# Kernel optimization log

Measured on AMD Instinct MI355X. Metric: run time of the kernel, lower is better.

## Reference

```python
import jax, jax.numpy as jnp
import numpy as np
import itertools

L, F, T = 16, 2, 2**19          # levels, features/level, hashmap size
BASE, SCALE = 16, 1.5           # base resolution, per-level scale
N = 524288                      # batch of sample points
PRIMES = np.array([1, 2654435761, 805459861, 3674653429], dtype=np.uint32)


def hash_encode(x, table):
    """Multi-resolution hash-grid encoding. x: [N,d] in [0,1); table: [L,T,F]."""
    n, d = x.shape
    corners = jnp.asarray(list(itertools.product([0, 1], repeat=d)), dtype=jnp.uint32)  # [C,d]
    primes = jnp.asarray(PRIMES[:d])
    is_hi = corners.astype(bool)[None]          # [1,C,d]
    outs = []
    for l in range(L):
        res = float(np.floor(BASE * SCALE**l))
        pos = x * res
        p0f = jnp.floor(pos)
        frac = pos - p0f                         # [N,d]
        p0 = p0f.astype(jnp.uint32)
        coords = p0[:, None, :] + corners[None]  # [N,C,d] uint32 (wraps)
        m = coords * primes                      # [N,C,d]
        h = m[..., 0]
        for j in range(1, d):
            h = h ^ m[..., j]
        idx = (h % np.uint32(T)).astype(jnp.int32)              # [N,C]
        w = jnp.where(is_hi, frac[:, None, :], 1.0 - frac[:, None, :]).prod(-1)  # [N,C]
        feat = table[l][idx]                                    # [N,C,F]
        outs.append(jnp.einsum('nc,ncf->nf', w, feat))
    return jnp.concatenate(outs, axis=-1)        # [N, L*F]


def mlp(h, w_in, w_hid, w_out):
    """tcnn-style bias-free MLP, ReLU hidden, linear output."""
    h = jax.nn.relu(h @ w_in)
    for i in range(w_hid.shape[0]):
        h = jax.nn.relu(h @ w_hid[i])
    return h @ w_out


def setup_inputs() -> dict:
    key = jax.random.key(0)
    ks = jax.random.split(key, 20)
    def w(k, shape):
        fan = shape[-2]
        return jax.random.normal(k, shape, jnp.float32) / np.sqrt(fan).astype(np.float32)
    return {
        'x': jax.random.uniform(ks[0], (N, 3), jnp.float32),
        't': jax.random.uniform(ks[1], (1,), jnp.float32),
        'skip_alpha': jax.random.uniform(ks[2], (1,), jnp.float32),
        'table_s': jax.random.normal(ks[3], (L, T, F), jnp.float32) * 1e-2,
        'ws_in': w(ks[4], (32, 64)),
        'ws_hid': w(ks[5], (3, 64, 64)),
        'ws_out': w(ks[6], (64, 64)),
        'table_d': jax.random.normal(ks[7], (L, T, F), jnp.float32) * 1e-2,
        'wd_in': w(ks[8], (32, 64)),
        'wd_hid': w(ks[9], (3, 64, 64)),
        'wd_out': w(ks[10], (64, 64)),
        'w1_in': w(ks[11], (128, 64)),
        'w1_hid': w(ks[12], (1, 64, 64)),
        'w1_out': w(ks[13], (64, 128)),
        'w2_in': w(ks[14], (128, 64)),
        'w2_hid': w(ks[15], (1, 64, 64)),
        'w2_out': w(ks[16], (64, 1)),
    }


def reference(x, t, skip_alpha, table_s, ws_in, ws_hid, ws_out,
              table_d, wd_in, wd_hid, wd_out,
              w1_in, w1_hid, w1_out, w2_in, w2_hid, w2_out):
    static_features = mlp(hash_encode(x, table_s), ws_in, ws_hid, ws_out)          # [N,64]
    t_col = jnp.broadcast_to(t, (x.shape[0], 1))
    x4 = jnp.concatenate([x, t_col], axis=1)                                        # [N,4]
    dynamic_features = mlp(hash_encode(x4, table_d), wd_in, wd_hid, wd_out)        # [N,64]
    features = jnp.concatenate([static_features, dynamic_features], axis=-1)       # [N,128]
    out1 = mlp(features, w1_in, w1_hid, w1_out)                                     # [N,128]
    blended = out1 * skip_alpha + (1.0 - skip_alpha) * features
    return mlp(blended, w2_in, w2_hid, w2_out)                                      # [N,1]
```

## Files before the change

### kernel.cpp

```cpp
#include <hip/hip_runtime.h>
#include <hip/hip_bf16.h>
#include <stdint.h>

#define LVLS 16
#define TSZ  524288
#define TMASK 0x7FFFFu
#define NPTS 524288
#define P1 2654435761u
#define P2 805459861u
#define P3 3674653429u

__constant__ float RES_TAB[16] = {
    16.f, 24.f, 36.f, 54.f, 81.f, 121.f, 182.f, 273.f,
    410.f, 615.f, 922.f, 1383.f, 2075.f, 3113.f, 4670.f, 7006.f};

using f16x8 = __attribute__((ext_vector_type(8))) _Float16;
using f32x4 = __attribute__((ext_vector_type(4))) float;
using u32x8 = __attribute__((ext_vector_type(8))) uint32_t;

union PackF16 { uint32_t u; _Float16 h[2]; };

constexpr int PS = 72;

struct WPtrs { const float* p[11]; };

__global__ void k_build(const float* __restrict__ ts, const float* __restrict__ td,
                        const float* __restrict__ tptr, uint2* __restrict__ Tc,
                        WPtrs wp, _Float16* __restrict__ wdst) {
    int B = blockIdx.x;
    int tid = threadIdx.x;
    if (B < 40960) {
        int c = B & 7, j = B >> 3;
        int l, i;
        if (j < 1024) {
            l = c >> 1;
            i = (c & 1) * 262144 + j * 256 + tid;
        } else if (j < 3072) {
            l = 12 + (c >> 1);
            i = (j - 1024) * 256 + tid;
        } else {
            l = 4 + c;
            i = (j - 3072) * 256 + tid;
        }
        int id = l * TSZ + i;
        float2 sv = ((const float2*)ts)[id];
        float res = RES_TAB[l];
        float tv  = tptr[0];
        float pt  = tv * res;
        float fpt = floorf(pt);
        float ft  = pt - fpt;
        uint32_t ut = (uint32_t)(int)fpt;
        uint32_t h0 = (ut * P3) & TMASK;
        uint32_t h1 = ((ut + 1u) * P3) & TMASK;
        const float2* tdl = (const float2*)td + (size_t)l * TSZ;
        float2 a = tdl[i ^ h0];
        float2 b = tdl[i ^ h1];
        PackF16 o0, o1;
        o0.h[0] = (_Float16)sv.x; o0.h[1] = (_Float16)sv.y;
        o1.h[0] = (_Float16)((1.f - ft) * a.x + ft * b.x);
        o1.h[1] = (_Float16)((1.f - ft) * a.y + ft * b.y);
        Tc[id] = make_uint2(o0.u, o1.u);
    } else {
        int id = (B - 40960) * 256 + tid;
        if (id >= 69632) return;
        const int OFF[16] = {0,2048,6144,10240,14336,18432,20480,24576,28672,
                             32768,36864,45056,49152,57344,65536,69632};
        const int KK[15]  = {32,64,64,64,64,32,64,64,64,64,128,64,64,128,64};
        const int NN[15]  = {64,64,64,64,64,64,64,64,64,64,64,64,128,64,64};
        const int PSEL[15]= {0,1,1,1,2,3,4,4,4,5,6,7,8,9,10};
        const int POFF[15]= {0,0,4096,8192,0,0,0,4096,8192,0,0,0,0,0,0};
        int m = 0;
        while (id >= OFF[m+1]) m++;
        int local = id - OFF[m];
        int jj   = local & 7;
        int lane = (local >> 3) & 63;
        int blk  = local >> 9;
        int KC   = KK[m] >> 5;
        int ct   = blk / KC;
        int kc   = blk - ct * KC;
        int k    = kc*32 + ((lane>>4)<<3) + jj;
        int n    = ct*16 + (lane & 15);
        const float* src = wp.p[PSEL[m]] + POFF[m];
        wdst[id] = (_Float16)src[k * NN[m] + n];
    }
}

__device__ __forceinline__ void gather1(const uint2* __restrict__ tcl,
                                        float px, float py, float pz,
                                        u32x8& va, u32x8& vb,
                                        float& wx, float& wy, float& wz) {
    float fx = floorf(px), fy = floorf(py), fz = floorf(pz);
    wx = px - fx; wy = py - fy; wz = pz - fz;
    uint32_t ux = (uint32_t)(int)fx, uy = (uint32_t)(int)fy, uz = (uint32_t)(int)fz;
    uint32_t hx0 = ux,     hx1 = ux + 1u;
    uint32_t hy0 = uy*P1,  hy1 = (uy+1u)*P1;
    uint32_t hz0 = uz*P2,  hz1 = (uz+1u)*P2;
#pragma unroll
    for (int cc = 0; cc < 8; cc++) {
        uint32_t idx = (((cc&1)?hx1:hx0) ^ ((cc&2)?hy1:hy0) ^ ((cc&4)?hz1:hz0)) & TMASK;
        uint2 t = tcl[idx];
        if (cc < 4) { va[(cc&3)*2+0] = t.x; va[(cc&3)*2+1] = t.y; }
        else        { vb[(cc&3)*2+0] = t.x; vb[(cc&3)*2+1] = t.y; }
    }
}

__device__ __forceinline__ void consume1(const u32x8& va, const u32x8& vb,
                                         float wx, float wy, float wz,
                                         uint32_t* __restrict__ es,
                                         uint32_t* __restrict__ ed, int p) {
    float wxa[2] = {1.f-wx, wx}, wya[2] = {1.f-wy, wy}, wza[2] = {1.f-wz, wz};
    float sA0 = 0.f, sA1 = 0.f, sD0 = 0.f, sD1 = 0.f;
#pragma unroll
    for (int cc = 0; cc < 8; cc++) {
        float w = wxa[cc&1] * wya[(cc>>1)&1] * wza[cc>>2];
        PackF16 s, d;
        s.u = (cc<4) ? va[(cc&3)*2+0] : vb[(cc&3)*2+0];
        d.u = (cc<4) ? va[(cc&3)*2+1] : vb[(cc&3)*2+1];
        sA0 += w*(float)s.h[0]; sA1 += w*(float)s.h[1];
        sD0 += w*(float)d.h[0]; sD1 += w*(float)d.h[1];
    }
    PackF16 o;
    o.h[0] = (_Float16)sA0; o.h[1] = (_Float16)sA1; es[p] = o.u;
    o.h[0] = (_Float16)sD0; o.h[1] = (_Float16)sD1; ed[p] = o.u;
}

#define MEMFENCE asm volatile("" ::: "memory")
#define PIN(a,b,c,d) asm volatile("" : "+v"(a), "+v"(b), "+v"(c), "+v"(d))

__launch_bounds__(256, 4)
__global__ void k_encode(const float* __restrict__ x,
                         const uint2* __restrict__ Tc,
                         uint32_t* __restrict__ EncS, uint32_t* __restrict__ EncD) {
    int tid = threadIdx.x;
    int c   = blockIdx.x & 7;
    int b   = blockIdx.x >> 3;
    int l, pb, stride;
    if (b < 256) {
        l = 4 + c;
        pb = b * 256 + tid;
        stride = 65536;
    } else if (b < 384) {
        l = 12 + (c >> 1);
        pb = (c & 1) * 262144 + (b - 256) * 256 + tid;
        stride = 32768;
    } else {
        l = c >> 1;
        pb = (c & 1) * 262144 + (b - 384) * 256 + tid;
        stride = 32768;
    }
    const uint2* tcl = Tc + (size_t)l * TSZ;
    uint32_t* es = EncS + (size_t)l * NPTS;
    uint32_t* ed = EncD + (size_t)l * NPTS;
    float res = RES_TAB[l];

    float PX[8], PY[8], PZ[8];
#pragma unroll
    for (int i = 0; i < 8; i++) {
        int p = pb + i * stride;
        PX[i] = x[p*3+0]*res; PY[i] = x[p*3+1]*res; PZ[i] = x[p*3+2]*res;
    }

    u32x8 A0, A1, A2, A3, B0, B1, B2, B3;
    float wA0x, wA0y, wA0z, wA1x, wA1y, wA1z;
    float wB0x, wB0y, wB0z, wB1x, wB1y, wB1z;

    gather1(tcl, PX[0], PY[0], PZ[0], A0, A1, wA0x, wA0y, wA0z);
    gather1(tcl, PX[1], PY[1], PZ[1], A2, A3, wA1x, wA1y, wA1z);
    gather1(tcl, PX[2], PY[2], PZ[2], B0, B1, wB0x, wB0y, wB0z);
    gather1(tcl, PX[3], PY[3], PZ[3], B2, B3, wB1x, wB1y, wB1z);
    MEMFENCE;
    PIN(A0, A1, A2, A3);
    consume1(A0, A1, wA0x, wA0y, wA0z, es, ed, pb + 0*stride);
    consume1(A2, A3, wA1x, wA1y, wA1z, es, ed, pb + 1*stride);
    gather1(tcl, PX[4], PY[4], PZ[4], A0, A1, wA0x, wA0y, wA0z);
    gather1(tcl, PX[5], PY[5], PZ[5], A2, A3, wA1x, wA1y, wA1z);
    MEMFENCE;
    PIN(B0, B1, B2, B3);
    consume1(B0, B1, wB0x, wB0y, wB0z, es, ed, pb + 2*stride);
    consume1(B2, B3, wB1x, wB1y, wB1z, es, ed, pb + 3*stride);
    gather1(tcl, PX[6], PY[6], PZ[6], B0, B1, wB0x, wB0y, wB0z);
    gather1(tcl, PX[7], PY[7], PZ[7], B2, B3, wB1x, wB1y, wB1z);
    MEMFENCE;
    PIN(A0, A1, A2, A3);
    consume1(A0, A1, wA0x, wA0y, wA0z, es, ed, pb + 4*stride);
    consume1(A2, A3, wA1x, wA1y, wA1z, es, ed, pb + 5*stride);
    PIN(B0, B1, B2, B3);
    consume1(B0, B1, wB0x, wB0y, wB0z, es, ed, pb + 6*stride);
    consume1(B2, B3, wB1x, wB1y, wB1z, es, ed, pb + 7*stride);
}

__device__ __forceinline__ void wait_lds() {
    asm volatile("s_waitcnt lgkmcnt(0)" ::: "memory");
}

template<int KC, bool RELU>
__device__ __forceinline__ void mm2(const f16x8 a[2][4], const f16x8* __restrict__ B,
                                    _Float16* dst, int m, int quad, int lane) {
#pragma unroll
    for (int ct = 0; ct < 4; ct++) {
        f32x4 acc0 = {0.f,0.f,0.f,0.f}, acc1 = {0.f,0.f,0.f,0.f};
#pragma unroll
        for (int kc = 0; kc < KC; kc++) {
            f16x8 b = B[(ct*KC+kc)*64 + lane];
            acc0 = __builtin_amdgcn_mfma_f32_16x16x32_f16(a[0][kc], b, acc0, 0, 0, 0);
            acc1 = __builtin_amdgcn_mfma_f32_16x16x32_f16(a[1][kc], b, acc1, 0, 0, 0);
        }
#pragma unroll
        for (int i = 0; i < 4; i++) {
            float v0 = acc0[i], v1 = acc1[i];
            if (RELU) { v0 = fmaxf(v0, 0.f); v1 = fmaxf(v1, 0.f); }
            dst[(0*16 + quad*4+i)*PS + ct*16 + m] = (_Float16)v0;
            dst[(1*16 + quad*4+i)*PS + ct*16 + m] = (_Float16)v1;
        }
    }
}

template<int KC>
__device__ __forceinline__ void mm2_keep(const f16x8 a[2][4], const f16x8* __restrict__ B,
                                         _Float16* dst, PackF16 P[2][8],
                                         int m, int quad, int lane) {
#pragma unroll
    for (int ct = 0; ct < 4; ct++) {
        f32x4 acc0 = {0.f,0.f,0.f,0.f}, acc1 = {0.f,0.f,0.f,0.f};
#pragma unroll
        for (int kc = 0; kc < KC; kc++) {
            f16x8 b = B[(ct*KC+kc)*64 + lane];
            acc0 = __builtin_amdgcn_mfma_f32_16x16x32_f16(a[0][kc], b, acc0, 0, 0, 0);
            acc1 = __builtin_amdgcn_mfma_f32_16x16x32_f16(a[1][kc], b, acc1, 0, 0, 0);
        }
#pragma unroll
        for (int ih = 0; ih < 2; ih++) {
            PackF16 p0, p1;
            p0.h[0] = (_Float16)acc0[ih*2+0]; p0.h[1] = (_Float16)acc0[ih*2+1];
            p1.h[0] = (_Float16)acc1[ih*2+0]; p1.h[1] = (_Float16)acc1[ih*2+1];
            P[0][ct*2+ih] = p0; P[1][ct*2+ih] = p1;
            dst[(0*16 + quad*4+ih*2+0)*PS + ct*16 + m] = p0.h[0];
            dst[(0*16 + quad*4+ih*2+1)*PS + ct*16 + m] = p0.h[1];
            dst[(1*16 + quad*4+ih*2+0)*PS + ct*16 + m] = p1.h[0];
            dst[(1*16 + quad*4+ih*2+1)*PS + ct*16 + m] = p1.h[1];
        }
    }
}

template<int KC>
__device__ __forceinline__ void read_a(const _Float16* buf, f16x8 a[2][4], int m, int quad) {
#pragma unroll
    for (int rt = 0; rt < 2; rt++)
#pragma unroll
        for (int kc = 0; kc < KC; kc++)
            a[rt][kc] = *(const f16x8*)(buf + (rt*16 + m)*PS + kc*32 + quad*8);
}

__device__ __forceinline__ void read_a128(const _Float16* Fs, const _Float16* Fd,
                                          f16x8 a[2][4], int m, int quad) {
#pragma unroll
    for (int rt = 0; rt < 2; rt++) {
#pragma unroll
        for (int kc = 0; kc < 2; kc++) {
            a[rt][kc]   = *(const f16x8*)(Fs + (rt*16 + m)*PS + kc*32 + quad*8);
            a[rt][kc+2] = *(const f16x8*)(Fd + (rt*16 + m)*PS + kc*32 + quad*8);
        }
    }
}

__device__ __forceinline__ void load_enc(const uint32_t* __restrict__ Enc,
                                         int pbase, int m, int quad, f16x8 a[2][4]) {
#pragma unroll
    for (int rt = 0; rt < 2; rt++) {
        union { uint32_t u[4]; f16x8 v; } cv;
        int p = pbase + rt*16 + m;
#pragma unroll
        for (int j = 0; j < 4; j++)
            cv.u[j] = Enc[(size_t)(quad*4 + j) * NPTS + p];
        a[rt][0] = cv.v;
    }
}

__launch_bounds__(256, 4)
__global__ void k_mlp(const uint32_t* __restrict__ EncS, const uint32_t* __restrict__ EncD,
                      const _Float16* __restrict__ Wfrag, const float* __restrict__ alphap,
                      const float* __restrict__ w2out, float* __restrict__ out) {
    __shared__ _Float16 FsB[4][32*PS];
    __shared__ _Float16 FdB[4][32*PS];
    int tid  = threadIdx.x;
    int wave = tid >> 6, lane = tid & 63;
    int m = lane & 15, quad = lane >> 4;
    int pbase = blockIdx.x * 128 + wave * 32;
    _Float16* Fs = FsB[wave];
    _Float16* Fd = FdB[wave];
    const f16x8* W8 = (const f16x8*)Wfrag;
    float alpha = alphap[0];

    f16x8 a[2][4];
    PackF16 sP[2][8], dP[2][8];

    load_enc(EncS, pbase, m, quad, a);
    mm2<1, true>(a, W8 + 0,    Fs, m, quad, lane); wait_lds();
    read_a<2>(Fs, a, m, quad);
    mm2<2, true>(a, W8 + 256,  Fs, m, quad, lane); wait_lds();
    read_a<2>(Fs, a, m, quad);
    mm2<2, true>(a, W8 + 768,  Fs, m, quad, lane); wait_lds();
    read_a<2>(Fs, a, m, quad);
    mm2<2, true>(a, W8 + 1280, Fs, m, quad, lane); wait_lds();
    read_a<2>(Fs, a, m, quad);
    mm2_keep<2>(a, W8 + 1792, Fs, sP, m, quad, lane);
    load_enc(EncD, pbase, m, quad, a);
    mm2<1, true>(a, W8 + 2304, Fd, m, quad, lane); wait_lds();
    read_a<2>(Fd, a, m, quad);
    mm2<2, true>(a, W8 + 2560, Fd, m, quad, lane); wait_lds();
    read_a<2>(Fd, a, m, quad);
    mm2<2, true>(a, W8 + 3072, Fd, m, quad, lane); wait_lds();
    read_a<2>(Fd, a, m, quad);
    mm2<2, true>(a, W8 + 3584, Fd, m, quad, lane); wait_lds();
    read_a<2>(Fd, a, m, quad);
    mm2_keep<2>(a, W8 + 4096, Fd, dP, m, quad, lane); wait_lds();
    read_a128(Fs, Fd, a, m, quad);
    mm2<4, true>(a, W8 + 4608, Fs, m, quad, lane); wait_lds();
    read_a<2>(Fs, a, m, quad);
    mm2<2, true>(a, W8 + 5632, Fs, m, quad, lane); wait_lds();
    read_a<2>(Fs, a, m, quad);
#pragma unroll
    for (int ct = 0; ct < 8; ct++) {
        f32x4 acc0 = {0.f,0.f,0.f,0.f}, acc1 = {0.f,0.f,0.f,0.f};
#pragma unroll
        for (int kc = 0; kc < 2; kc++) {
            f16x8 b = W8[6144 + (ct*2+kc)*64 + lane];
            acc0 = __builtin_amdgcn_mfma_f32_16x16x32_f16(a[0][kc], b, acc0, 0, 0, 0);
            acc1 = __builtin_amdgcn_mfma_f32_16x16x32_f16(a[1][kc], b, acc1, 0, 0, 0);
        }
        _Float16* tgt = (ct < 4) ? Fs : Fd;
        int col = (ct & 3) * 16 + m;
#pragma unroll
        for (int i = 0; i < 4; i++) {
            float f0 = (ct < 4) ? (float)sP[0][ct*2 + (i>>1)].h[i&1]
                                : (float)dP[0][(ct-4)*2 + (i>>1)].h[i&1];
            float f1 = (ct < 4) ? (float)sP[1][ct*2 + (i>>1)].h[i&1]
                                : (float)dP[1][(ct-4)*2 + (i>>1)].h[i&1];
            tgt[(0*16 + quad*4+i)*PS + col] = (_Float16)(alpha*acc0[i] + (1.f-alpha)*f0);
            tgt[(1*16 + quad*4+i)*PS + col] = (_Float16)(alpha*acc1[i] + (1.f-alpha)*f1);
        }
    }
    wait_lds();
    read_a128(Fs, Fd, a, m, quad);
    mm2<4, true>(a, W8 + 7168, Fs, m, quad, lane); wait_lds();
    read_a<2>(Fs, a, m, quad);
    float rsum0[4] = {0.f,0.f,0.f,0.f}, rsum1[4] = {0.f,0.f,0.f,0.f};
#pragma unroll
    for (int ct = 0; ct < 4; ct++) {
        f32x4 acc0 = {0.f,0.f,0.f,0.f}, acc1 = {0.f,0.f,0.f,0.f};
#pragma unroll
        for (int kc = 0; kc < 2; kc++) {
            f16x8 b = W8[8192 + (ct*2+kc)*64 + lane];
            acc0 = __builtin_amdgcn_mfma_f32_16x16x32_f16(a[0][kc], b, acc0, 0, 0, 0);
            acc1 = __builtin_amdgcn_mfma_f32_16x16x32_f16(a[1][kc], b, acc1, 0, 0, 0);
        }
        float wv = w2out[ct*16 + m];
#pragma unroll
        for (int i = 0; i < 4; i++) {
            rsum0[i] += fmaxf(acc0[i], 0.f) * wv;
            rsum1[i] += fmaxf(acc1[i], 0.f) * wv;
        }
    }
#pragma unroll
    for (int off = 1; off < 16; off <<= 1) {
#pragma unroll
        for (int i = 0; i < 4; i++) {
            rsum0[i] += __shfl_xor(rsum0[i], off, 64);
            rsum1[i] += __shfl_xor(rsum1[i], off, 64);
        }
    }
    if (m == 0) {
#pragma unroll
        for (int i = 0; i < 4; i++) {
            out[pbase + 0*16 + quad*4 + i] = rsum0[i];
            out[pbase + 1*16 + quad*4 + i] = rsum1[i];
        }
    }
}

extern "C" void kernel_launch(void* const* d_in, const int* in_sizes, int n_in,
                              void* d_out, int out_size, void* d_ws, size_t ws_size,
                              hipStream_t stream) {
    const float* x      = (const float*)d_in[0];
    const float* t      = (const float*)d_in[1];
    const float* alpha  = (const float*)d_in[2];
    const float* tab_s  = (const float*)d_in[3];
    const float* ws_in  = (const float*)d_in[4];
    const float* ws_hid = (const float*)d_in[5];
    const float* ws_out = (const float*)d_in[6];
    const float* tab_d  = (const float*)d_in[7];
    const float* wd_in  = (const float*)d_in[8];
    const float* wd_hid = (const float*)d_in[9];
    const float* wd_out = (const float*)d_in[10];
    const float* w1_in  = (const float*)d_in[11];
    const float* w1_hid = (const float*)d_in[12];
    const float* w1_out = (const float*)d_in[13];
    const float* w2_in  = (const float*)d_in[14];
    const float* w2_hid = (const float*)d_in[15];
    const float* w2_out = (const float*)d_in[16];
    float* out = (float*)d_out;

    char* ws = (char*)d_ws;
    _Float16* Wfrag = (_Float16*)ws;
    uint2*    Tc    = (uint2*)(ws + 139264);
    uint32_t* EncS  = (uint32_t*)(ws + 139264 + 67108864);
    uint32_t* EncD  = EncS + (size_t)LVLS * NPTS;
    size_t needed = 139264 + 67108864 + 2ull * 33554432ull;
    if (ws_size < needed) return;

    WPtrs wp;
    wp.p[0] = ws_in;  wp.p[1] = ws_hid; wp.p[2] = ws_out;
    wp.p[3] = wd_in;  wp.p[4] = wd_hid; wp.p[5] = wd_out;
    wp.p[6] = w1_in;  wp.p[7] = w1_hid; wp.p[8] = w1_out;
    wp.p[9] = w2_in;  wp.p[10] = w2_hid;

    k_build  <<<41232, 256, 0, stream>>>(tab_s, tab_d, t, Tc, wp, Wfrag);
    k_encode <<<4096,  256, 0, stream>>>(x, Tc, EncS, EncD);
    k_mlp    <<<NPTS/128, 256, 0, stream>>>(EncS, EncD, Wfrag, alpha, w2_out, out);
}
```

Baseline: 545.9 us.

## Pair x-adjacent hash corners into 16-byte loads with a three-deep gather pipeline

The encode gather now uses the fact that the x-neighbour corners differ only in the low hash bits. When ux is even, the two x-corners land in the same aligned 16-byte pair, so one uint4 load fetches both. When ux is odd, four extra 8-byte loads are issued. The software pipeline also changes from batches of 2+2 points to a rotating three-slot schedule, with x coordinates loaded inside each issue. This cuts load instructions and transactions for about half the points, at the cost of divergent branches on x-parity and extra select logic.

```diff
diff --git a/kernel.cpp b/kernel.cpp
--- a/kernel.cpp
+++ b/kernel.cpp
@@ -85,47 +85,86 @@
     }
 }
 
-__device__ __forceinline__ void gather1(const uint2* __restrict__ tcl,
-                                        float px, float py, float pz,
-                                        u32x8& va, u32x8& vb,
-                                        float& wx, float& wy, float& wz) {
+#define MEMFENCE asm volatile("" ::: "memory")
+#define PIN3(a,b,c) asm volatile("" : "+v"(a), "+v"(b), "+v"(c))
+
+__device__ __forceinline__ void issueP(const float* __restrict__ x,
+                                       const uint2* __restrict__ tcl, float res,
+                                       int p,
+                                       u32x8& vp0, u32x8& vp1, u32x8& vo,
+                                       float& wx, float& wy, float& wz,
+                                       uint32_t& sel, uint32_t& par) {
+    float px = x[p*3+0]*res, py = x[p*3+1]*res, pz = x[p*3+2]*res;
     float fx = floorf(px), fy = floorf(py), fz = floorf(pz);
-    wx = px - fx; wy = py - fy; wz = pz - fz;
+    wx = px-fx; wy = py-fy; wz = pz-fz;
     uint32_t ux = (uint32_t)(int)fx, uy = (uint32_t)(int)fy, uz = (uint32_t)(int)fz;
-    uint32_t hx0 = ux,     hx1 = ux + 1u;
-    uint32_t hy0 = uy*P1,  hy1 = (uy+1u)*P1;
-    uint32_t hz0 = uz*P2,  hz1 = (uz+1u)*P2;
-#pragma unroll
-    for (int cc = 0; cc < 8; cc++) {
-        uint32_t idx = (((cc&1)?hx1:hx0) ^ ((cc&2)?hy1:hy0) ^ ((cc&4)?hz1:hz0)) & TMASK;
-        uint2 t = tcl[idx];
-        if (cc < 4) { va[(cc&3)*2+0] = t.x; va[(cc&3)*2+1] = t.y; }
-        else        { vb[(cc&3)*2+0] = t.x; vb[(cc&3)*2+1] = t.y; }
-    }
-}
-
-__device__ __forceinline__ void consume1(const u32x8& va, const u32x8& vb,
+    uint32_t hy0 = uy*P1, hy1 = (uy+1u)*P1;
+    uint32_t hz0 = uz*P2, hz1 = (uz+1u)*P2;
+    par = ux & 1u;
+    if (par) {
+#pragma unroll
+        for (int d = 0; d < 4; d++) {
+            uint32_t r  = ((d&1) ? hy1 : hy0) ^ ((d>>1) ? hz1 : hz0);
+            uint32_t i1 = ((ux + 1u) ^ r) & TMASK;
+            uint2 t = tcl[i1];
+            vo[d*2+0] = t.x; vo[d*2+1] = t.y;
+        }
+    }
+    uint32_t s = 0;
+#pragma unroll
+    for (int d = 0; d < 4; d++) {
+        uint32_t r  = ((d&1) ? hy1 : hy0) ^ ((d>>1) ? hz1 : hz0);
+        uint32_t i0 = (ux ^ r) & TMASK;
+        s |= (i0 & 1u) << d;
+        const uint32_t* src = (const uint32_t*)tcl + (size_t)(i0 & ~1u) * 2u;
+        uint4 t = *(const uint4*)src;
+        if (d < 2) {
+            vp0[(d&1)*4+0] = t.x; vp0[(d&1)*4+1] = t.y;
+            vp0[(d&1)*4+2] = t.z; vp0[(d&1)*4+3] = t.w;
+        } else {
+            vp1[(d&1)*4+0] = t.x; vp1[(d&1)*4+1] = t.y;
+            vp1[(d&1)*4+2] = t.z; vp1[(d&1)*4+3] = t.w;
+        }
+    }
+    sel = s;
+}
+
+__device__ __forceinline__ void consumeP(const u32x8& vp0, const u32x8& vp1,
+                                         const u32x8& vo,
                                          float wx, float wy, float wz,
+                                         uint32_t sel, uint32_t par,
                                          uint32_t* __restrict__ es,
                                          uint32_t* __restrict__ ed, int p) {
     float wxa[2] = {1.f-wx, wx}, wya[2] = {1.f-wy, wy}, wza[2] = {1.f-wz, wz};
     float sA0 = 0.f, sA1 = 0.f, sD0 = 0.f, sD1 = 0.f;
-#pragma unroll
-    for (int cc = 0; cc < 8; cc++) {
-        float w = wxa[cc&1] * wya[(cc>>1)&1] * wza[cc>>2];
-        PackF16 s, d;
-        s.u = (cc<4) ? va[(cc&3)*2+0] : vb[(cc&3)*2+0];
-        d.u = (cc<4) ? va[(cc&3)*2+1] : vb[(cc&3)*2+1];
-        sA0 += w*(float)s.h[0]; sA1 += w*(float)s.h[1];
-        sD0 += w*(float)d.h[0]; sD1 += w*(float)d.h[1];
+    bool odd = (par != 0u);
+#pragma unroll
+    for (int d = 0; d < 4; d++) {
+        uint32_t h0 = (sel >> d) & 1u;
+        const int e = (d&1)*4;
+        uint32_t lo0 = (d<2) ? vp0[e+0] : vp1[e+0];
+        uint32_t lo1 = (d<2) ? vp0[e+1] : vp1[e+1];
+        uint32_t hi0 = (d<2) ? vp0[e+2] : vp1[e+2];
+        uint32_t hi1 = (d<2) ? vp0[e+3] : vp1[e+3];
+        uint32_t a0 = h0 ? hi0 : lo0;
+        uint32_t a1 = h0 ? hi1 : lo1;
+        uint32_t p0w = h0 ? lo0 : hi0;
+        uint32_t p1w = h0 ? lo1 : hi1;
+        uint32_t b0 = odd ? vo[d*2+0] : p0w;
+        uint32_t b1 = odd ? vo[d*2+1] : p1w;
+        float wyz = wya[d&1] * wza[d>>1];
+        float w0 = wxa[0]*wyz, w1 = wxa[1]*wyz;
+        PackF16 s0, d0, s1, d1;
+        s0.u = a0; d0.u = a1; s1.u = b0; d1.u = b1;
+        sA0 += w0*(float)s0.h[0] + w1*(float)s1.h[0];
+        sA1 += w0*(float)s0.h[1] + w1*(float)s1.h[1];
+        sD0 += w0*(float)d0.h[0] + w1*(float)d1.h[0];
+        sD1 += w0*(float)d0.h[1] + w1*(float)d1.h[1];
     }
     PackF16 o;
     o.h[0] = (_Float16)sA0; o.h[1] = (_Float16)sA1; es[p] = o.u;
     o.h[0] = (_Float16)sD0; o.h[1] = (_Float16)sD1; ed[p] = o.u;
 }
-
-#define MEMFENCE asm volatile("" ::: "memory")
-#define PIN(a,b,c,d) asm volatile("" : "+v"(a), "+v"(b), "+v"(c), "+v"(d))
 
 __launch_bounds__(256, 4)
 __global__ void k_encode(const float* __restrict__ x,
@@ -153,40 +192,41 @@
     uint32_t* ed = EncD + (size_t)l * NPTS;
     float res = RES_TAB[l];
 
-    float PX[8], PY[8], PZ[8];
-#pragma unroll
-    for (int i = 0; i < 8; i++) {
-        int p = pb + i * stride;
-        PX[i] = x[p*3+0]*res; PY[i] = x[p*3+1]*res; PZ[i] = x[p*3+2]*res;
-    }
-
-    u32x8 A0, A1, A2, A3, B0, B1, B2, B3;
-    float wA0x, wA0y, wA0z, wA1x, wA1y, wA1z;
-    float wB0x, wB0y, wB0z, wB1x, wB1y, wB1z;
-
-    gather1(tcl, PX[0], PY[0], PZ[0], A0, A1, wA0x, wA0y, wA0z);
-    gather1(tcl, PX[1], PY[1], PZ[1], A2, A3, wA1x, wA1y, wA1z);
-    gather1(tcl, PX[2], PY[2], PZ[2], B0, B1, wB0x, wB0y, wB0z);
-    gather1(tcl, PX[3], PY[3], PZ[3], B2, B3, wB1x, wB1y, wB1z);
-    MEMFENCE;
-    PIN(A0, A1, A2, A3);
-    consume1(A0, A1, wA0x, wA0y, wA0z, es, ed, pb + 0*stride);
-    consume1(A2, A3, wA1x, wA1y, wA1z, es, ed, pb + 1*stride);
-    gather1(tcl, PX[4], PY[4], PZ[4], A0, A1, wA0x, wA0y, wA0z);
-    gather1(tcl, PX[5], PY[5], PZ[5], A2, A3, wA1x, wA1y, wA1z);
-    MEMFENCE;
-    PIN(B0, B1, B2, B3);
-    consume1(B0, B1, wB0x, wB0y, wB0z, es, ed, pb + 2*stride);
-    consume1(B2, B3, wB1x, wB1y, wB1z, es, ed, pb + 3*stride);
-    gather1(tcl, PX[6], PY[6], PZ[6], B0, B1, wB0x, wB0y, wB0z);
-    gather1(tcl, PX[7], PY[7], PZ[7], B2, B3, wB1x, wB1y, wB1z);
-    MEMFENCE;
-    PIN(A0, A1, A2, A3);
-    consume1(A0, A1, wA0x, wA0y, wA0z, es, ed, pb + 4*stride);
-    consume1(A2, A3, wA1x, wA1y, wA1z, es, ed, pb + 5*stride);
-    PIN(B0, B1, B2, B3);
-    consume1(B0, B1, wB0x, wB0y, wB0z, es, ed, pb + 6*stride);
-    consume1(B2, B3, wB1x, wB1y, wB1z, es, ed, pb + 7*stride);
+    u32x8 pA0, pA1, pB0, pB1, pC0, pC1;
+    u32x8 oA = {}, oB = {}, oC = {};
+    float wAx, wAy, wAz, wBx, wBy, wBz, wCx, wCy, wCz;
+    uint32_t selA, parA, selB, parB, selC, parC;
+
+    issueP(x, tcl, res, pb + 0*stride, pA0, pA1, oA, wAx, wAy, wAz, selA, parA);
+    issueP(x, tcl, res, pb + 1*stride, pB0, pB1, oB, wBx, wBy, wBz, selB, parB);
+    issueP(x, tcl, res, pb + 2*stride, pC0, pC1, oC, wCx, wCy, wCz, selC, parC);
+    MEMFENCE;
+    PIN3(pA0, pA1, oA);
+    consumeP(pA0, pA1, oA, wAx, wAy, wAz, selA, parA, es, ed, pb + 0*stride);
+    issueP(x, tcl, res, pb + 3*stride, pA0, pA1, oA, wAx, wAy, wAz, selA, parA);
+    MEMFENCE;
+    PIN3(pB0, pB1, oB);
+    consumeP(pB0, pB1, oB, wBx, wBy, wBz, selB, parB, es, ed, pb + 1*stride);
+    issueP(x, tcl, res, pb + 4*stride, pB0, pB1, oB, wBx, wBy, wBz, selB, parB);
+    MEMFENCE;
+    PIN3(pC0, pC1, oC);
+    consumeP(pC0, pC1, oC, wCx, wCy, wCz, selC, parC, es, ed, pb + 2*stride);
+    issueP(x, tcl, res, pb + 5*stride, pC0, pC1, oC, wCx, wCy, wCz, selC, parC);
+    MEMFENCE;
+    PIN3(pA0, pA1, oA);
+    consumeP(pA0, pA1, oA, wAx, wAy, wAz, selA, parA, es, ed, pb + 3*stride);
+    issueP(x, tcl, res, pb + 6*stride, pA0, pA1, oA, wAx, wAy, wAz, selA, parA);
+    MEMFENCE;
+    PIN3(pB0, pB1, oB);
+    consumeP(pB0, pB1, oB, wBx, wBy, wBz, selB, parB, es, ed, pb + 4*stride);
+    issueP(x, tcl, res, pb + 7*stride, pB0, pB1, oB, wBx, wBy, wBz, selB, parB);
+    MEMFENCE;
+    PIN3(pC0, pC1, oC);
+    consumeP(pC0, pC1, oC, wCx, wCy, wCz, selC, parC, es, ed, pb + 5*stride);
+    PIN3(pA0, pA1, oA);
+    consumeP(pA0, pA1, oA, wAx, wAy, wAz, selA, parA, es, ed, pb + 6*stride);
+    PIN3(pB0, pB1, oB);
+    consumeP(pB0, pB1, oB, wBx, wBy, wBz, selB, parB, es, ed, pb + 7*stride);
 }
 
 __device__ __forceinline__ void wait_lds() {
```

Result: slower. 560.8 us (+2.7%).

## Process 64 rows per wave in MLP kernel to reuse weight fragments

Applied to the files above, without the earlier changes.

Each wave now computes four 16-row tiles (64 points) instead of two, so every weight fragment load from global/L2 feeds four MFMAs instead of two. Blocks shrink to two waves of 128 threads, keeping 128 points per block, and per-wave LDS buffers double to 64 rows. This halves weight-fragment traffic per point but raises register pressure (a[4][4], sP/dP[4][8], four accumulators), which may cut occupancy or cause spills.

```diff
diff --git a/kernel.cpp b/kernel.cpp
--- a/kernel.cpp
+++ b/kernel.cpp
@@ -194,67 +194,76 @@
 }
 
 template<int KC, bool RELU>
-__device__ __forceinline__ void mm2(const f16x8 a[2][4], const f16x8* __restrict__ B,
+__device__ __forceinline__ void mm2(const f16x8 a[4][4], const f16x8* __restrict__ B,
                                     _Float16* dst, int m, int quad, int lane) {
+    const f32x4 zero = {0.f,0.f,0.f,0.f};
 #pragma unroll
     for (int ct = 0; ct < 4; ct++) {
-        f32x4 acc0 = {0.f,0.f,0.f,0.f}, acc1 = {0.f,0.f,0.f,0.f};
+        f32x4 acc[4];
+#pragma unroll
+        for (int rt = 0; rt < 4; rt++) acc[rt] = zero;
 #pragma unroll
         for (int kc = 0; kc < KC; kc++) {
             f16x8 b = B[(ct*KC+kc)*64 + lane];
-            acc0 = __builtin_amdgcn_mfma_f32_16x16x32_f16(a[0][kc], b, acc0, 0, 0, 0);
-            acc1 = __builtin_amdgcn_mfma_f32_16x16x32_f16(a[1][kc], b, acc1, 0, 0, 0);
-        }
-#pragma unroll
-        for (int i = 0; i < 4; i++) {
-            float v0 = acc0[i], v1 = acc1[i];
-            if (RELU) { v0 = fmaxf(v0, 0.f); v1 = fmaxf(v1, 0.f); }
-            dst[(0*16 + quad*4+i)*PS + ct*16 + m] = (_Float16)v0;
-            dst[(1*16 + quad*4+i)*PS + ct*16 + m] = (_Float16)v1;
-        }
+#pragma unroll
+            for (int rt = 0; rt < 4; rt++)
+                acc[rt] = __builtin_amdgcn_mfma_f32_16x16x32_f16(a[rt][kc], b, acc[rt], 0, 0, 0);
+        }
+#pragma unroll
+        for (int rt = 0; rt < 4; rt++)
+#pragma unroll
+            for (int i = 0; i < 4; i++) {
+                float v = acc[rt][i];
+                if (RELU) v = fmaxf(v, 0.f);
+                dst[(rt*16 + quad*4+i)*PS + ct*16 + m] = (_Float16)v;
+            }
     }
 }
 
 template<int KC>
-__device__ __forceinline__ void mm2_keep(const f16x8 a[2][4], const f16x8* __restrict__ B,
-                                         _Float16* dst, PackF16 P[2][8],
+__device__ __forceinline__ void mm2_keep(const f16x8 a[4][4], const f16x8* __restrict__ B,
+                                         _Float16* dst, PackF16 P[4][8],
                                          int m, int quad, int lane) {
+    const f32x4 zero = {0.f,0.f,0.f,0.f};
 #pragma unroll
     for (int ct = 0; ct < 4; ct++) {
-        f32x4 acc0 = {0.f,0.f,0.f,0.f}, acc1 = {0.f,0.f,0.f,0.f};
+        f32x4 acc[4];
+#pragma unroll
+        for (int rt = 0; rt < 4; rt++) acc[rt] = zero;
 #pragma unroll
         for (int kc = 0; kc < KC; kc++) {
             f16x8 b = B[(ct*KC+kc)*64 + lane];
-            acc0 = __builtin_amdgcn_mfma_f32_16x16x32_f16(a[0][kc], b, acc0, 0, 0, 0);
-            acc1 = __builtin_amdgcn_mfma_f32_16x16x32_f16(a[1][kc], b, acc1, 0, 0, 0);
-        }
-#pragma unroll
-        for (int ih = 0; ih < 2; ih++) {
-            PackF16 p0, p1;
-            p0.h[0] = (_Float16)acc0[ih*2+0]; p0.h[1] = (_Float16)acc0[ih*2+1];
-            p1.h[0] = (_Float16)acc1[ih*2+0]; p1.h[1] = (_Float16)acc1[ih*2+1];
-            P[0][ct*2+ih] = p0; P[1][ct*2+ih] = p1;
-            dst[(0*16 + quad*4+ih*2+0)*PS + ct*16 + m] = p0.h[0];
-            dst[(0*16 + quad*4+ih*2+1)*PS + ct*16 + m] = p0.h[1];
-            dst[(1*16 + quad*4+ih*2+0)*PS + ct*16 + m] = p1.h[0];
-            dst[(1*16 + quad*4+ih*2+1)*PS + ct*16 + m] = p1.h[1];
-        }
+#pragma unroll
+            for (int rt = 0; rt < 4; rt++)
+                acc[rt] = __builtin_amdgcn_mfma_f32_16x16x32_f16(a[rt][kc], b, acc[rt], 0, 0, 0);
+        }
+#pragma unroll
+        for (int rt = 0; rt < 4; rt++)
+#pragma unroll
+            for (int ih = 0; ih < 2; ih++) {
+                PackF16 p0;
+                p0.h[0] = (_Float16)acc[rt][ih*2+0];
+                p0.h[1] = (_Float16)acc[rt][ih*2+1];
+                P[rt][ct*2+ih] = p0;
+                dst[(rt*16 + quad*4+ih*2+0)*PS + ct*16 + m] = p0.h[0];
+                dst[(rt*16 + quad*4+ih*2+1)*PS + ct*16 + m] = p0.h[1];
+            }
     }
 }
 
 template<int KC>
-__device__ __forceinline__ void read_a(const _Float16* buf, f16x8 a[2][4], int m, int quad) {
-#pragma unroll
-    for (int rt = 0; rt < 2; rt++)
+__device__ __forceinline__ void read_a(const _Float16* buf, f16x8 a[4][4], int m, int quad) {
+#pragma unroll
+    for (int rt = 0; rt < 4; rt++)
 #pragma unroll
         for (int kc = 0; kc < KC; kc++)
             a[rt][kc] = *(const f16x8*)(buf + (rt*16 + m)*PS + kc*32 + quad*8);
 }
 
 __device__ __forceinline__ void read_a128(const _Float16* Fs, const _Float16* Fd,
-                                          f16x8 a[2][4], int m, int quad) {
-#pragma unroll
-    for (int rt = 0; rt < 2; rt++) {
+                                          f16x8 a[4][4], int m, int quad) {
+#pragma unroll
+    for (int rt = 0; rt < 4; rt++) {
 #pragma unroll
         for (int kc = 0; kc < 2; kc++) {
             a[rt][kc]   = *(const f16x8*)(Fs + (rt*16 + m)*PS + kc*32 + quad*8);
@@ -264,9 +273,9 @@
 }
 
 __device__ __forceinline__ void load_enc(const uint32_t* __restrict__ Enc,
-                                         int pbase, int m, int quad, f16x8 a[2][4]) {
-#pragma unroll
-    for (int rt = 0; rt < 2; rt++) {
+                                         int pbase, int m, int quad, f16x8 a[4][4]) {
+#pragma unroll
+    for (int rt = 0; rt < 4; rt++) {
         union { uint32_t u[4]; f16x8 v; } cv;
         int p = pbase + rt*16 + m;
 #pragma unroll
@@ -276,23 +285,23 @@
     }
 }
 
-__launch_bounds__(256, 4)
+__launch_bounds__(128, 2)
 __global__ void k_mlp(const uint32_t* __restrict__ EncS, const uint32_t* __restrict__ EncD,
                       const _Float16* __restrict__ Wfrag, const float* __restrict__ alphap,
                       const float* __restrict__ w2out, float* __restrict__ out) {
-    __shared__ _Float16 FsB[4][32*PS];
-    __shared__ _Float16 FdB[4][32*PS];
+    __shared__ _Float16 FsB[2][64*PS];
+    __shared__ _Float16 FdB[2][64*PS];
     int tid  = threadIdx.x;
     int wave = tid >> 6, lane = tid & 63;
     int m = lane & 15, quad = lane >> 4;
-    int pbase = blockIdx.x * 128 + wave * 32;
+    int pbase = blockIdx.x * 128 + wave * 64;
     _Float16* Fs = FsB[wave];
     _Float16* Fd = FdB[wave];
     const f16x8* W8 = (const f16x8*)Wfrag;
     float alpha = alphap[0];
 
-    f16x8 a[2][4];
-    PackF16 sP[2][8], dP[2][8];
+    f16x8 a[4][4];
+    PackF16 sP[4][8], dP[4][8];
 
     load_enc(EncS, pbase, m, quad, a);
     mm2<1, true>(a, W8 + 0,    Fs, m, quad, lane); wait_lds();
@@ -319,62 +328,74 @@
     read_a<2>(Fs, a, m, quad);
     mm2<2, true>(a, W8 + 5632, Fs, m, quad, lane); wait_lds();
     read_a<2>(Fs, a, m, quad);
-#pragma unroll
-    for (int ct = 0; ct < 8; ct++) {
-        f32x4 acc0 = {0.f,0.f,0.f,0.f}, acc1 = {0.f,0.f,0.f,0.f};
-#pragma unroll
-        for (int kc = 0; kc < 2; kc++) {
-            f16x8 b = W8[6144 + (ct*2+kc)*64 + lane];
-            acc0 = __builtin_amdgcn_mfma_f32_16x16x32_f16(a[0][kc], b, acc0, 0, 0, 0);
-            acc1 = __builtin_amdgcn_mfma_f32_16x16x32_f16(a[1][kc], b, acc1, 0, 0, 0);
-        }
-        _Float16* tgt = (ct < 4) ? Fs : Fd;
-        int col = (ct & 3) * 16 + m;
-#pragma unroll
-        for (int i = 0; i < 4; i++) {
-            float f0 = (ct < 4) ? (float)sP[0][ct*2 + (i>>1)].h[i&1]
-                                : (float)dP[0][(ct-4)*2 + (i>>1)].h[i&1];
-            float f1 = (ct < 4) ? (float)sP[1][ct*2 + (i>>1)].h[i&1]
-                                : (float)dP[1][(ct-4)*2 + (i>>1)].h[i&1];
-            tgt[(0*16 + quad*4+i)*PS + col] = (_Float16)(alpha*acc0[i] + (1.f-alpha)*f0);
-            tgt[(1*16 + quad*4+i)*PS + col] = (_Float16)(alpha*acc1[i] + (1.f-alpha)*f1);
+    {
+        const f32x4 zero = {0.f,0.f,0.f,0.f};
+#pragma unroll
+        for (int ct = 0; ct < 8; ct++) {
+            f32x4 acc[4];
+#pragma unroll
+            for (int rt = 0; rt < 4; rt++) acc[rt] = zero;
+#pragma unroll
+            for (int kc = 0; kc < 2; kc++) {
+                f16x8 b = W8[6144 + (ct*2+kc)*64 + lane];
+#pragma unroll
+                for (int rt = 0; rt < 4; rt++)
+                    acc[rt] = __builtin_amdgcn_mfma_f32_16x16x32_f16(a[rt][kc], b, acc[rt], 0, 0, 0);
+            }
+            _Float16* tgt = (ct < 4) ? Fs : Fd;
+            int col = (ct & 3) * 16 + m;
+#pragma unroll
+            for (int rt = 0; rt < 4; rt++)
+#pragma unroll
+                for (int i = 0; i < 4; i++) {
+                    float f = (ct < 4) ? (float)sP[rt][ct*2 + (i>>1)].h[i&1]
+                                       : (float)dP[rt][(ct-4)*2 + (i>>1)].h[i&1];
+                    tgt[(rt*16 + quad*4+i)*PS + col] = (_Float16)(alpha*acc[rt][i] + (1.f-alpha)*f);
+                }
         }
     }
     wait_lds();
     read_a128(Fs, Fd, a, m, quad);
     mm2<4, true>(a, W8 + 7168, Fs, m, quad, lane); wait_lds();
     read_a<2>(Fs, a, m, quad);
-    float rsum0[4] = {0.f,0.f,0.f,0.f}, rsum1[4] = {0.f,0.f,0.f,0.f};
-#pragma unroll
-    for (int ct = 0; ct < 4; ct++) {
-        f32x4 acc0 = {0.f,0.f,0.f,0.f}, acc1 = {0.f,0.f,0.f,0.f};
-#pragma unroll
-        for (int kc = 0; kc < 2; kc++) {
-            f16x8 b = W8[8192 + (ct*2+kc)*64 + lane];
-            acc0 = __builtin_amdgcn_mfma_f32_16x16x32_f16(a[0][kc], b, acc0, 0, 0, 0);
-            acc1 = __builtin_amdgcn_mfma_f32_16x16x32_f16(a[1][kc], b, acc1, 0, 0, 0);
-        }
-        float wv = w2out[ct*16 + m];
-#pragma unroll
-        for (int i = 0; i < 4; i++) {
-            rsum0[i] += fmaxf(acc0[i], 0.f) * wv;
-            rsum1[i] += fmaxf(acc1[i], 0.f) * wv;
+    float rsum[4][4] = {{0.f,0.f,0.f,0.f},{0.f,0.f,0.f,0.f},
+                        {0.f,0.f,0.f,0.f},{0.f,0.f,0.f,0.f}};
+    {
+        const f32x4 zero = {0.f,0.f,0.f,0.f};
+#pragma unroll
+        for (int ct = 0; ct < 4; ct++) {
+            f32x4 acc[4];
+#pragma unroll
+            for (int rt = 0; rt < 4; rt++) acc[rt] = zero;
+#pragma unroll
+            for (int kc = 0; kc < 2; kc++) {
+                f16x8 b = W8[8192 + (ct*2+kc)*64 + lane];
+#pragma unroll
+                for (int rt = 0; rt < 4; rt++)
+                    acc[rt] = __builtin_amdgcn_mfma_f32_16x16x32_f16(a[rt][kc], b, acc[rt], 0, 0, 0);
+            }
+            float wv = w2out[ct*16 + m];
+#pragma unroll
+            for (int rt = 0; rt < 4; rt++)
+#pragma unroll
+                for (int i = 0; i < 4; i++)
+                    rsum[rt][i] += fmaxf(acc[rt][i], 0.f) * wv;
         }
     }
 #pragma unroll
     for (int off = 1; off < 16; off <<= 1) {
 #pragma unroll
-        for (int i = 0; i < 4; i++) {
-            rsum0[i] += __shfl_xor(rsum0[i], off, 64);
-            rsum1[i] += __shfl_xor(rsum1[i], off, 64);
-        }
+        for (int rt = 0; rt < 4; rt++)
+#pragma unroll
+            for (int i = 0; i < 4; i++)
+                rsum[rt][i] += __shfl_xor(rsum[rt][i], off, 64);
     }
     if (m == 0) {
 #pragma unroll
-        for (int i = 0; i < 4; i++) {
-            out[pbase + 0*16 + quad*4 + i] = rsum0[i];
-            out[pbase + 1*16 + quad*4 + i] = rsum1[i];
-        }
+        for (int rt = 0; rt < 4; rt++)
+#pragma unroll
+            for (int i = 0; i < 4; i++)
+                out[pbase + rt*16 + quad*4 + i] = rsum[rt][i];
     }
 }
 
@@ -416,5 +437,5 @@
 
     k_build  <<<41232, 256, 0, stream>>>(tab_s, tab_d, t, Tc, wp, Wfrag);
     k_encode <<<4096,  256, 0, stream>>>(x, Tc, EncS, EncD);
-    k_mlp    <<<NPTS/128, 256, 0, stream>>>(EncS, EncD, Wfrag, alpha, w2_out, out);
-}
+    k_mlp    <<<NPTS/128, 128, 0, stream>>>(EncS, EncD, Wfrag, alpha, w2_out, out);
+}
```

New measurement: 561.0 us. 1.03x slower.
